# Kernel optimization log

Measured on AMD Instinct MI355X. Metric: run time of the kernel, lower is better.

## Reference

```python
import jax, jax.numpy as jnp
import numpy as np

B = 16384          # batch_size (z_i rows)
D = 2048           # latent_size
PRIOR = 0.3
PRIOR_PRIME = 0.5
GAMMA = 1.0
BETA = 0.0


def setup_inputs() -> dict:
    key = jax.random.key(0)
    k1, k2, k3, k4 = jax.random.split(key, 4)
    z_i = jax.random.normal(k1, (B, D), dtype=jnp.float32)
    z_j = jax.random.normal(k2, (B, D), dtype=jnp.float32)
    # nn.Linear(latent_size, 1): weight (1, D) stored flat as (D,), bias scalar
    W = jax.random.normal(k3, (D,), dtype=jnp.float32) / np.sqrt(D)
    b = jax.random.normal(k4, (), dtype=jnp.float32) * 0.01
    return {"z_i": z_i, "z_j": z_j, "W": W, "b": b}


def reference(z_i, z_j, W, b):
    # pred = flatten(Linear(cat(z_i, z_j)))  -> (2B,)
    z = jnp.concatenate([z_i, z_j], axis=0)
    pred = z @ W + b                        # (n,) with n = 2B
    n = pred.shape[0]
    batch = n // 2
    # targets matrix: -1 everywhere, +1 on diagonal and at the (i, i+B)/(i+B, i)
    # contrastive pairs -> each row i has exactly 2 positives: i and pair(i).
    idx = jnp.arange(batch)
    pair = jnp.concatenate([idx + batch, idx])   # pair(i) for every row i
    s_pos = jax.nn.sigmoid(pred)    # loss_func(-x) = sigmoid(x)
    s_neg = jax.nn.sigmoid(-pred)   # loss_func(x)  = sigmoid(-x)
    # per-row sums of the onnpu_loss (row i of targets used as target vector)
    sum_y_pos = s_neg + s_neg[pair]                 # sum(loss(pos*inp)*pos)
    sum_y_pos_inv = s_pos + s_pos[pair]             # sum(loss(-pos*inp)*pos)
    total_s_pos = jnp.sum(s_pos)
    sum_y_unl = total_s_pos - s_pos - s_pos[pair]   # sum(loss(-unl*inp)*unl)
    n_positive = jnp.maximum(1.0, 2.0)              # max(min_count, 2)
    n_unlabeled = jnp.maximum(1.0, jnp.float32(n) - 2.0)
    positive_risk = PRIOR_PRIME / n_positive * sum_y_pos
    negative_risk = ((1.0 - PRIOR_PRIME) / (n_unlabeled * (1.0 - PRIOR)) * sum_y_unl
                     - (1.0 - PRIOR_PRIME) * PRIOR / (n_positive * (1.0 - PRIOR)) * sum_y_pos_inv)
    # nnPU branch: if negative_risk < -beta -> -gamma * negative_risk
    loss_rows = jnp.where(negative_risk < -BETA,
                          -GAMMA * negative_risk,
                          positive_risk + negative_risk)
    return jnp.mean(loss_rows)
```

## Files before the change

kernel.cpp:

```cpp
#include <hip/hip_runtime.h>
#include <math.h>

#define B_ROWS 16384
#define DLAT   2048
#define NTOT   (2 * B_ROWS)
#define NPART  (NTOT / 4)

__global__ __launch_bounds__(256) void k_dot_sig(
    const float* __restrict__ zi, const float* __restrict__ zj,
    const float* __restrict__ W,  const float* __restrict__ bptr,
    float* __restrict__ sp, float* __restrict__ partial)
{
    const int wave = threadIdx.x >> 6;
    const int lane = threadIdx.x & 63;
    const int row  = blockIdx.x * 4 + wave;

    const float* zrow = (row < B_ROWS)
        ? (zi + (size_t)row * DLAT)
        : (zj + (size_t)(row - B_ROWS) * DLAT);

    const float4* z4 = (const float4*)zrow;
    const float4* w4 = (const float4*)W;

    float acc = 0.0f;
    #pragma unroll
    for (int it = 0; it < 8; ++it) {
        float4 z = z4[it * 64 + lane];
        float4 w = w4[it * 64 + lane];
        acc += z.x * w.x + z.y * w.y + z.z * w.z + z.w * w.w;
    }

    #pragma unroll
    for (int off = 32; off > 0; off >>= 1)
        acc += __shfl_xor(acc, off, 64);

    __shared__ float s4[4];
    if (lane == 0) {
        float pred = acc + bptr[0];
        float spv  = 1.0f / (1.0f + expf(-pred));
        sp[row]  = spv;
        s4[wave] = spv;
    }
    __syncthreads();
    if (threadIdx.x == 0)
        partial[blockIdx.x] = (s4[0] + s4[1]) + (s4[2] + s4[3]);
}

__global__ __launch_bounds__(1024) void k_finish(
    const float* __restrict__ sp, const float* __restrict__ partial,
    float* __restrict__ out)
{
    __shared__ float red[1024];
    const int t = threadIdx.x;

    float tot = 0.0f;
    for (int i = t; i < NPART; i += 1024) tot += partial[i];
    red[t] = tot;
    __syncthreads();
    #pragma unroll
    for (int s = 512; s > 0; s >>= 1) {
        if (t < s) red[t] += red[t + s];
        __syncthreads();
    }
    const float total_s_pos = red[0];
    __syncthreads();

    const float c1 = 0.5f / (((float)NTOT - 2.0f) * 0.7f);
    const float c2 = (0.5f * 0.3f) / (2.0f * 0.7f);

    float lsum = 0.0f;
    for (int r = t; r < NTOT; r += 1024) {
        float S2  = sp[r] + sp[r ^ B_ROWS];
        float pos = 0.25f * (2.0f - S2);
        float neg = c1 * (total_s_pos - S2) - c2 * S2;
        lsum += (neg < 0.0f) ? -neg : (pos + neg);
    }
    red[t] = lsum;
    __syncthreads();
    #pragma unroll
    for (int s = 512; s > 0; s >>= 1) {
        if (t < s) red[t] += red[t + s];
        __syncthreads();
    }
    if (t == 0) out[0] = red[0] / (float)NTOT;
}

extern "C" void kernel_launch(void* const* d_in, const int* in_sizes, int n_in,
                              void* d_out, int out_size, void* d_ws, size_t ws_size,
                              hipStream_t stream) {
    const float* zi = (const float*)d_in[0];
    const float* zj = (const float*)d_in[1];
    const float* W  = (const float*)d_in[2];
    const float* b  = (const float*)d_in[3];

    float* sp      = (float*)d_ws;
    float* partial = sp + NTOT;
    float* out     = (float*)d_out;

    k_dot_sig<<<NTOT / 4, 256, 0, stream>>>(zi, zj, W, b, sp, partial);
    k_finish<<<1, 1024, 0, stream>>>(sp, partial, out);
}
```

Measured before the change: 284.1 us.

## Process two rows per wave with upfront loads and parallelize final loss reduction

The dot-product kernel now has each wave handle two rows. All sixteen float4 row loads are issued before the multiply, so more memory requests are in flight and each W load is reused across two rows. The single-block finish kernel is split into three launches: a total reduction, a 128-block per-row loss stage, and a final mean. This spreads the 32K-row loss pass across many CUs but adds two extra kernel launches, and the workload is dominated by streaming 256MB of input.

Measured after the change: 280.3 us. About the same (-1.4%).

```diff
diff --git a/kernel.cpp b/kernel.cpp
--- a/kernel.cpp
+++ b/kernel.cpp
@@ -4,82 +4,113 @@
 #define B_ROWS 16384
 #define DLAT   2048
 #define NTOT   (2 * B_ROWS)
-#define NPART  (NTOT / 4)
+#define NBLK1  (NTOT / 8)
+#define NBLK3  128
 
-__global__ __launch_bounds__(256) void k_dot_sig(
+__global__ __launch_bounds__(256, 4) void k_dot_sig(
     const float* __restrict__ zi, const float* __restrict__ zj,
     const float* __restrict__ W,  const float* __restrict__ bptr,
     float* __restrict__ sp, float* __restrict__ partial)
 {
-    const int wave = threadIdx.x >> 6;
     const int lane = threadIdx.x & 63;
-    const int row  = blockIdx.x * 4 + wave;
+    const int wv   = threadIdx.x >> 6;
+    const int r0   = (blockIdx.x * 4 + wv) * 2;
+    const int r1   = r0 + 1;
 
-    const float* zrow = (row < B_ROWS)
-        ? (zi + (size_t)row * DLAT)
-        : (zj + (size_t)(row - B_ROWS) * DLAT);
+    const float4* pa = (const float4*)((r0 < B_ROWS)
+        ? zi + (size_t)r0 * DLAT : zj + (size_t)(r0 - B_ROWS) * DLAT);
+    const float4* pb = (const float4*)((r1 < B_ROWS)
+        ? zi + (size_t)r1 * DLAT : zj + (size_t)(r1 - B_ROWS) * DLAT);
 
-    const float4* z4 = (const float4*)zrow;
+    float4 za[8], zb[8];
+    #pragma unroll
+    for (int i = 0; i < 8; ++i) za[i] = pa[i * 64 + lane];
+    #pragma unroll
+    for (int i = 0; i < 8; ++i) zb[i] = pb[i * 64 + lane];
+
     const float4* w4 = (const float4*)W;
-
-    float acc = 0.0f;
+    float aA = 0.0f, aB = 0.0f;
     #pragma unroll
-    for (int it = 0; it < 8; ++it) {
-        float4 z = z4[it * 64 + lane];
-        float4 w = w4[it * 64 + lane];
-        acc += z.x * w.x + z.y * w.y + z.z * w.z + z.w * w.w;
+    for (int i = 0; i < 8; ++i) {
+        float4 w = w4[i * 64 + lane];
+        aA += za[i].x * w.x + za[i].y * w.y + za[i].z * w.z + za[i].w * w.w;
+        aB += zb[i].x * w.x + zb[i].y * w.y + zb[i].z * w.z + zb[i].w * w.w;
     }
 
     #pragma unroll
-    for (int off = 32; off > 0; off >>= 1)
-        acc += __shfl_xor(acc, off, 64);
+    for (int off = 32; off > 0; off >>= 1) {
+        aA += __shfl_xor(aA, off, 64);
+        aB += __shfl_xor(aB, off, 64);
+    }
 
-    __shared__ float s4[4];
+    __shared__ float s8[8];
     if (lane == 0) {
-        float pred = acc + bptr[0];
-        float spv  = 1.0f / (1.0f + expf(-pred));
-        sp[row]  = spv;
-        s4[wave] = spv;
+        float b  = bptr[0];
+        float sA = 1.0f / (1.0f + expf(-(aA + b)));
+        float sB = 1.0f / (1.0f + expf(-(aB + b)));
+        sp[r0] = sA; sp[r1] = sB;
+        s8[wv * 2] = sA; s8[wv * 2 + 1] = sB;
     }
     __syncthreads();
     if (threadIdx.x == 0)
-        partial[blockIdx.x] = (s4[0] + s4[1]) + (s4[2] + s4[3]);
+        partial[blockIdx.x] = ((s8[0] + s8[1]) + (s8[2] + s8[3]))
+                            + ((s8[4] + s8[5]) + (s8[6] + s8[7]));
 }
 
-__global__ __launch_bounds__(1024) void k_finish(
-    const float* __restrict__ sp, const float* __restrict__ partial,
-    float* __restrict__ out)
+__global__ __launch_bounds__(1024) void k_total(
+    const float* __restrict__ partial, float* __restrict__ total)
 {
     __shared__ float red[1024];
     const int t = threadIdx.x;
-
-    float tot = 0.0f;
-    for (int i = t; i < NPART; i += 1024) tot += partial[i];
-    red[t] = tot;
+    float s = 0.0f;
+    for (int i = t; i < NBLK1; i += 1024) s += partial[i];
+    red[t] = s;
     __syncthreads();
     #pragma unroll
-    for (int s = 512; s > 0; s >>= 1) {
-        if (t < s) red[t] += red[t + s];
+    for (int st = 512; st > 0; st >>= 1) {
+        if (t < st) red[t] += red[t + st];
         __syncthreads();
     }
-    const float total_s_pos = red[0];
-    __syncthreads();
+    if (t == 0) total[0] = red[0];
+}
 
-    const float c1 = 0.5f / (((float)NTOT - 2.0f) * 0.7f);
-    const float c2 = (0.5f * 0.3f) / (2.0f * 0.7f);
+__global__ __launch_bounds__(256) void k_loss(
+    const float* __restrict__ sp, const float* __restrict__ total,
+    float* __restrict__ lp)
+{
+    const int t = threadIdx.x;
+    const int r = blockIdx.x * 256 + t;
 
-    float lsum = 0.0f;
-    for (int r = t; r < NTOT; r += 1024) {
-        float S2  = sp[r] + sp[r ^ B_ROWS];
-        float pos = 0.25f * (2.0f - S2);
-        float neg = c1 * (total_s_pos - S2) - c2 * S2;
-        lsum += (neg < 0.0f) ? -neg : (pos + neg);
-    }
-    red[t] = lsum;
+    const float tot = total[0];
+    const float c1  = 0.5f / (((float)NTOT - 2.0f) * 0.7f);
+    const float c2  = (0.5f * 0.3f) / (2.0f * 0.7f);
+
+    float S2  = sp[r] + sp[r ^ B_ROWS];
+    float pos = 0.25f * (2.0f - S2);
+    float neg = c1 * (tot - S2) - c2 * S2;
+    float l   = (neg < 0.0f) ? -neg : (pos + neg);
+
+    __shared__ float red[256];
+    red[t] = l;
     __syncthreads();
     #pragma unroll
-    for (int s = 512; s > 0; s >>= 1) {
-        if (t < s) red[t] += red[t + s];
+    for (int st = 128; st > 0; st >>= 1) {
+        if (t < st) red[t] += red[t + st];
+        __syncthreads();
+    }
+    if (t == 0) lp[blockIdx.x] = red[0];
+}
+
+__global__ __launch_bounds__(128) void k_mean(
+    const float* __restrict__ lp, float* __restrict__ out)
+{
+    __shared__ float red[128];
+    const int t = threadIdx.x;
+    red[t] = lp[t];
+    __syncthreads();
+    #pragma unroll
+    for (int st = 64; st > 0; st >>= 1) {
+        if (t < st) red[t] += red[t + st];
         __syncthreads();
     }
     if (t == 0) out[0] = red[0] / (float)NTOT;
@@ -95,8 +126,12 @@
 
     float* sp      = (float*)d_ws;
     float* partial = sp + NTOT;
+    float* lp      = partial + NBLK1;
+    float* total   = lp + NBLK3;
     float* out     = (float*)d_out;
 
-    k_dot_sig<<<NTOT / 4, 256, 0, stream>>>(zi, zj, W, b, sp, partial);
-    k_finish<<<1, 1024, 0, stream>>>(sp, partial, out);
+    k_dot_sig<<<NBLK1, 256, 0, stream>>>(zi, zj, W, b, sp, partial);
+    k_total <<<1, 1024, 0, stream>>>(partial, total);
+    k_loss  <<<NBLK3, 256, 0, stream>>>(sp, total, lp);
+    k_mean  <<<1, 128, 0, stream>>>(lp, out);
 }
```
